# Optimization experiments

Hardware: AMD Instinct MI355X
Metric: run time of the kernel (lower is better)

The kernel has to match this reference:

```python
import jax, jax.numpy as jnp
import numpy as np

B, N, E, FIN, FOUT = 4, 50000, 800000, 128, 64
ALPHA = 0.2  # LeakyReLU negative slope
NEG_BIG = -9e15


def setup_inputs() -> dict:
    key = jax.random.key(0)
    kx, kw, ka, ksrc, kdst = jax.random.split(key, 5)
    X = jax.random.normal(kx, (B, N, FIN), dtype=jnp.float32)
    W = jax.random.normal(kw, (FIN, FOUT), dtype=jnp.float32) * 0.1
    a = jax.random.normal(ka, (1, 2 * FOUT), dtype=jnp.float32) * 0.1
    # edges [B,2,E]; guarantee every row (destination of aggregation) has >=1 edge
    # so e_rowsum > 0 (mirrors real adjacency which has self-loops / connectivity).
    src_rand = jax.random.randint(ksrc, (B, E - N), 0, N, dtype=jnp.int32)
    src = jnp.concatenate(
        [jnp.broadcast_to(jnp.arange(N, dtype=jnp.int32), (B, N)), src_rand], axis=1
    )
    dst = jax.random.randint(kdst, (B, E), 0, N, dtype=jnp.int32)
    edges = jnp.stack([src, dst], axis=1)  # [B,2,E]
    return {"X": X, "edges": edges, "W": W, "a": a}


def _per_graph(x, edge, W, a):
    # x: [N,FIN], edge: [2,E]
    h = x @ W                                   # [N,FOUT]
    a1, a2 = a[0, :FOUT], a[0, FOUT:]           # split a . concat(h_i,h_j)
    s = (h @ a1)[edge[0]] + (h @ a2)[edge[1]]   # [E] attention logits
    edge_e = jnp.exp(-jax.nn.leaky_relu(s, ALPHA))          # [E]
    rowsum = jax.ops.segment_sum(edge_e, edge[0], num_segments=N)  # [N]
    msg = edge_e[:, None] * h[edge[1]]          # [E,FOUT]
    h_prime = jax.ops.segment_sum(msg, edge[0], num_segments=N)    # [N,FOUT]
    h_prime = h_prime / rowsum[:, None]
    h_prime = jnp.where(jnp.isnan(h_prime), jnp.float32(NEG_BIG), h_prime)
    return h_prime


def reference(X, edges, W, a):
    out = jax.vmap(_per_graph, in_axes=(0, 0, None, None))(X, edges, W, a)  # [B,N,FOUT]
    return jax.nn.elu(out)  # concat=True path
```

## Files before the change

### kernel.cpp

```cpp
#include <hip/hip_runtime.h>

#define B_    4
#define N_    50000
#define E_    800000
#define FIN_  128
#define F_    64
#define BN_   (B_ * N_)
#define TOT_  (BN_ * F_)
#define BE_   (B_ * E_)
#define ALPHA_ 0.2f
#define NEG_BIG_ -9.0e15f

#define XS_STRIDE 132
#define GEMM_BLOCKS (BN_ / 64)
#define COUNT_BLOCKS (BE_ / 1024)

#define MAXDEG_ 28
#define OVFCAP_ 16384

__device__ __forceinline__ float bf2f(unsigned int u16) {
    union { unsigned int i; float f; } v;
    v.i = u16 << 16;
    return v.f;
}
__device__ __forceinline__ unsigned int f2bf(float f) {
    union { float f; unsigned int u; } v;
    v.f = f;
    unsigned int r = v.u + 0x7FFFu + ((v.u >> 16) & 1u);
    return r >> 16;
}

__global__ __launch_bounds__(256) void gemm_count_kernel(
    const float* __restrict__ X,
    const float* __restrict__ W,
    const float* __restrict__ a,
    const int* __restrict__ edges,
    unsigned short* __restrict__ hq,
    float* __restrict__ e1,
    float* __restrict__ e2,
    int* __restrict__ cnt,
    int* __restrict__ ell,
    int* __restrict__ ovfc,
    int2* __restrict__ ovf) {
    __shared__ float Wf[FIN_ * F_];
    __shared__ float Xs[64 * XS_STRIDE];

    const int tid = threadIdx.x;
    const int bid = blockIdx.x;

    if (bid & 1) {
        const int g  = (bid >> 1) * 256 + tid;
        const int ge = g * 4;
        const int b  = ge / E_;
        const int e  = ge - b * E_;
        const int4 s4 = *(const int4*)&edges[(size_t)b * 2 * E_ + e];
        const int4 d4 = *(const int4*)&edges[(size_t)b * 2 * E_ + E_ + e];
        const int ss[4] = { s4.x, s4.y, s4.z, s4.w };
        const int dd[4] = { d4.x, d4.y, d4.z, d4.w };
#pragma unroll
        for (int j = 0; j < 4; ++j) {
            const int gs = b * N_ + ss[j];
            const int r = atomicAdd(&cnt[gs], 1);
            if (r < MAXDEG_) {
                ell[gs * MAXDEG_ + r] = dd[j];
            } else {
                const int i = atomicAdd(ovfc, 1);
                if (i < OVFCAP_) ovf[i] = make_int2(gs, dd[j]);
            }
        }
        return;
    }

    const float4* Wg = (const float4*)W;
    for (int i = tid; i < 2048; i += 256)
        ((float4*)Wf)[i] = Wg[i];

    const int row0 = (bid >> 1) * 64;
    const float4* Xg = (const float4*)(X + (size_t)row0 * FIN_);
    for (int i = tid; i < 2048; i += 256) {
        const int r = i >> 5;
        const int c = i & 31;
        float4 v = Xg[i];
        *(float4*)&Xs[r * XS_STRIDE + c * 4] = v;
    }
    __syncthreads();

    const int cg = tid & 15;
    const int rg = tid >> 4;

    float acc[4][4] = {};
#pragma unroll 4
    for (int k = 0; k < FIN_; ++k) {
        const float4 wv = *(const float4*)&Wf[k * F_ + cg * 4];
        float xr[4];
#pragma unroll
        for (int j = 0; j < 4; ++j)
            xr[j] = Xs[(rg * 4 + j) * XS_STRIDE + k];
#pragma unroll
        for (int j = 0; j < 4; ++j) {
            acc[j][0] += xr[j] * wv.x;
            acc[j][1] += xr[j] * wv.y;
            acc[j][2] += xr[j] * wv.z;
            acc[j][3] += xr[j] * wv.w;
        }
    }

    float a1v[4], a2v[4];
#pragma unroll
    for (int i = 0; i < 4; ++i) {
        a1v[i] = a[cg * 4 + i];
        a2v[i] = a[F_ + cg * 4 + i];
    }

#pragma unroll
    for (int j = 0; j < 4; ++j) {
        const int row = row0 + rg * 4 + j;
        union { ushort4 v; unsigned short s[4]; } st;
#pragma unroll
        for (int i = 0; i < 4; ++i) st.s[i] = (unsigned short)f2bf(acc[j][i]);
        *(ushort4*)&hq[(size_t)row * F_ + cg * 4] = st.v;

        float p1 = acc[j][0] * a1v[0] + acc[j][1] * a1v[1] +
                   acc[j][2] * a1v[2] + acc[j][3] * a1v[3];
        float p2 = acc[j][0] * a2v[0] + acc[j][1] * a2v[1] +
                   acc[j][2] * a2v[2] + acc[j][3] * a2v[3];
#pragma unroll
        for (int m = 8; m >= 1; m >>= 1) {
            p1 += __shfl_xor(p1, m);
            p2 += __shfl_xor(p2, m);
        }
        if (cg == 0) { e1[row] = p1; e2[row] = p2; }
    }
}

__global__ __launch_bounds__(256) void gather_kernel(
    const int* __restrict__ cnt,
    const int* __restrict__ ell,
    const int* __restrict__ ovfc,
    const int2* __restrict__ ovf,
    const float* __restrict__ e1,
    const float* __restrict__ e2,
    const uint4* __restrict__ hq4,
    float* __restrict__ out) {
    const int tid = threadIdx.x;
    const int lane = tid & 63;
    const int grp = lane >> 3;
    const int sub = lane & 7;
    const int gs = (int)((blockIdx.x * 256 + tid) >> 6);
    const int b = gs / N_;
    const uint4* hb = hq4 + (size_t)b * N_ * 8;
    const float* e2b = e2 + b * N_;
    const int cv = cnt[gs];
    const float e1s = e1[gs];
    const int deg = cv < MAXDEG_ ? cv : MAXDEG_;
    const int base = gs * MAXDEG_;

    const bool v0 = grp < deg;
    const bool v1 = grp + 8 < deg;
    const bool v2 = grp + 16 < deg;
    const bool v3 = (grp < 4) && (grp + 24 < deg);
    const int d0 = ell[base + grp];
    const int d1 = ell[base + grp + 8];
    const int d2 = ell[base + grp + 16];
    const int d3 = (grp < 4) ? ell[base + grp + 24] : 0;

    float a0 = 0.f, a1 = 0.f, a2 = 0.f, a3 = 0.f;
    float a4 = 0.f, a5 = 0.f, a6 = 0.f, a7 = 0.f, rs = 0.f;

#define GAT_SLOT(vld, dv)                                              \
    if (vld) {                                                         \
        const float sv = e1s + e2b[dv];                                \
        const float lr = sv > 0.0f ? sv : ALPHA_ * sv;                 \
        const float wt = __expf(-lr);                                  \
        const uint4 p = hb[(size_t)(dv) * 8 + sub];                    \
        a0 += wt * bf2f(p.x & 0xFFFFu); a1 += wt * bf2f(p.x >> 16);    \
        a2 += wt * bf2f(p.y & 0xFFFFu); a3 += wt * bf2f(p.y >> 16);    \
        a4 += wt * bf2f(p.z & 0xFFFFu); a5 += wt * bf2f(p.z >> 16);    \
        a6 += wt * bf2f(p.w & 0xFFFFu); a7 += wt * bf2f(p.w >> 16);    \
        rs += wt;                                                      \
    }

    GAT_SLOT(v0, d0)
    GAT_SLOT(v1, d1)
    GAT_SLOT(v2, d2)
    GAT_SLOT(v3, d3)
#undef GAT_SLOT

    if (cv > MAXDEG_) {
        int no = *ovfc;
        if (no > OVFCAP_) no = OVFCAP_;
        for (int i = 0; i < no; ++i) {
            const int2 t = ovf[i];
            if (t.x == gs) {
                const float sv = e1s + e2b[t.y];
                const float lr = sv > 0.0f ? sv : ALPHA_ * sv;
                const float wt = __expf(-lr);
                if (grp == 0) {
                    const uint4 p = hb[(size_t)t.y * 8 + sub];
                    a0 += wt * bf2f(p.x & 0xFFFFu); a1 += wt * bf2f(p.x >> 16);
                    a2 += wt * bf2f(p.y & 0xFFFFu); a3 += wt * bf2f(p.y >> 16);
                    a4 += wt * bf2f(p.z & 0xFFFFu); a5 += wt * bf2f(p.z >> 16);
                    a6 += wt * bf2f(p.w & 0xFFFFu); a7 += wt * bf2f(p.w >> 16);
                    rs += wt;
                }
            }
        }
    }

#pragma unroll
    for (int m = 8; m <= 32; m <<= 1) {
        a0 += __shfl_xor(a0, m); a1 += __shfl_xor(a1, m);
        a2 += __shfl_xor(a2, m); a3 += __shfl_xor(a3, m);
        a4 += __shfl_xor(a4, m); a5 += __shfl_xor(a5, m);
        a6 += __shfl_xor(a6, m); a7 += __shfl_xor(a7, m);
        rs += __shfl_xor(rs, m);
    }

    if (grp == 0) {
        float v[8] = { a0 / rs, a1 / rs, a2 / rs, a3 / rs,
                       a4 / rs, a5 / rs, a6 / rs, a7 / rs };
        float o[8];
#pragma unroll
        for (int j = 0; j < 8; ++j) {
            float x = v[j];
            if (x != x) x = NEG_BIG_;
            o[j] = x > 0.0f ? x : (__expf(x) - 1.0f);
        }
        float* po = &out[(size_t)gs * F_ + sub * 8];
        *(float4*)&po[0] = make_float4(o[0], o[1], o[2], o[3]);
        *(float4*)&po[4] = make_float4(o[4], o[5], o[6], o[7]);
    }
}

extern "C" void kernel_launch(void* const* d_in, const int* in_sizes, int n_in,
                              void* d_out, int out_size, void* d_ws, size_t ws_size,
                              hipStream_t stream) {
    const float* X = (const float*)d_in[0];
    const int* edges = (const int*)d_in[1];
    const float* W = (const float*)d_in[2];
    const float* a = (const float*)d_in[3];
    float* out = (float*)d_out;

    float* e1 = (float*)d_ws;
    float* e2 = e1 + BN_;
    unsigned short* hq = (unsigned short*)(e2 + BN_);
    int* cnt = (int*)(hq + (size_t)BN_ * F_);
    int* ovfc = cnt + BN_;
    int2* ovf = (int2*)(ovfc + 4);
    int* ell = (int*)(ovf + OVFCAP_);

    (void)hipMemsetAsync(cnt, 0, (size_t)(BN_ + 4) * sizeof(int), stream);

    gemm_count_kernel<<<GEMM_BLOCKS + COUNT_BLOCKS, 256, 0, stream>>>(
        X, W, a, edges, hq, e1, e2, cnt, ell, ovfc, ovf);
    gather_kernel<<<BN_ / 4, 256, 0, stream>>>(
        cnt, ell, ovfc, ovf, e1, e2, (const uint4*)hq, out);
}
```

Before: 427.4 us.

## Store ELL adjacency as 16-bit indices and issue gather loads unconditionally

The ELL neighbor list is narrowed from int to unsigned short, since N fits in 16 bits, which halves its write and read traffic. The ELL buffer is now zero-filled by the memset so that unused slots point to node 0. The gather kernel then loads all four slots and their h rows without branching and masks the weights to zero. The count path issues its four atomics back to back. In exchange, the memset grows (about 11 MB) and the gather makes extra useless loads for empty slots.

```diff
diff --git a/kernel.cpp b/kernel.cpp
--- a/kernel.cpp
+++ b/kernel.cpp
@@ -39,7 +39,7 @@
     float* __restrict__ e1,
     float* __restrict__ e2,
     int* __restrict__ cnt,
-    int* __restrict__ ell,
+    unsigned short* __restrict__ ell,
     int* __restrict__ ovfc,
     int2* __restrict__ ovf) {
     __shared__ float Wf[FIN_ * F_];
@@ -55,17 +55,21 @@
         const int e  = ge - b * E_;
         const int4 s4 = *(const int4*)&edges[(size_t)b * 2 * E_ + e];
         const int4 d4 = *(const int4*)&edges[(size_t)b * 2 * E_ + E_ + e];
-        const int ss[4] = { s4.x, s4.y, s4.z, s4.w };
+        const int gsv[4] = { b * N_ + s4.x, b * N_ + s4.y,
+                             b * N_ + s4.z, b * N_ + s4.w };
         const int dd[4] = { d4.x, d4.y, d4.z, d4.w };
+        int r[4];
+        r[0] = atomicAdd(&cnt[gsv[0]], 1);
+        r[1] = atomicAdd(&cnt[gsv[1]], 1);
+        r[2] = atomicAdd(&cnt[gsv[2]], 1);
+        r[3] = atomicAdd(&cnt[gsv[3]], 1);
 #pragma unroll
         for (int j = 0; j < 4; ++j) {
-            const int gs = b * N_ + ss[j];
-            const int r = atomicAdd(&cnt[gs], 1);
-            if (r < MAXDEG_) {
-                ell[gs * MAXDEG_ + r] = dd[j];
+            if (r[j] < MAXDEG_) {
+                ell[(size_t)gsv[j] * MAXDEG_ + r[j]] = (unsigned short)dd[j];
             } else {
                 const int i = atomicAdd(ovfc, 1);
-                if (i < OVFCAP_) ovf[i] = make_int2(gs, dd[j]);
+                if (i < OVFCAP_) ovf[i] = make_int2(gsv[j], dd[j]);
             }
         }
         return;
@@ -133,9 +137,20 @@
     }
 }
 
+struct Acc9 {
+    float a0, a1, a2, a3, a4, a5, a6, a7, rs;
+    __device__ __forceinline__ void add(float wt, const uint4& p) {
+        a0 += wt * bf2f(p.x & 0xFFFFu); a1 += wt * bf2f(p.x >> 16);
+        a2 += wt * bf2f(p.y & 0xFFFFu); a3 += wt * bf2f(p.y >> 16);
+        a4 += wt * bf2f(p.z & 0xFFFFu); a5 += wt * bf2f(p.z >> 16);
+        a6 += wt * bf2f(p.w & 0xFFFFu); a7 += wt * bf2f(p.w >> 16);
+        rs += wt;
+    }
+};
+
 __global__ __launch_bounds__(256) void gather_kernel(
     const int* __restrict__ cnt,
-    const int* __restrict__ ell,
+    const unsigned short* __restrict__ ell,
     const int* __restrict__ ovfc,
     const int2* __restrict__ ovf,
     const float* __restrict__ e1,
@@ -152,39 +167,37 @@
     const float* e2b = e2 + b * N_;
     const int cv = cnt[gs];
     const float e1s = e1[gs];
-    const int deg = cv < MAXDEG_ ? cv : MAXDEG_;
-    const int base = gs * MAXDEG_;
-
-    const bool v0 = grp < deg;
-    const bool v1 = grp + 8 < deg;
-    const bool v2 = grp + 16 < deg;
-    const bool v3 = (grp < 4) && (grp + 24 < deg);
-    const int d0 = ell[base + grp];
-    const int d1 = ell[base + grp + 8];
-    const int d2 = ell[base + grp + 16];
-    const int d3 = (grp < 4) ? ell[base + grp + 24] : 0;
-
-    float a0 = 0.f, a1 = 0.f, a2 = 0.f, a3 = 0.f;
-    float a4 = 0.f, a5 = 0.f, a6 = 0.f, a7 = 0.f, rs = 0.f;
-
-#define GAT_SLOT(vld, dv)                                              \
-    if (vld) {                                                         \
-        const float sv = e1s + e2b[dv];                                \
-        const float lr = sv > 0.0f ? sv : ALPHA_ * sv;                 \
-        const float wt = __expf(-lr);                                  \
-        const uint4 p = hb[(size_t)(dv) * 8 + sub];                    \
-        a0 += wt * bf2f(p.x & 0xFFFFu); a1 += wt * bf2f(p.x >> 16);    \
-        a2 += wt * bf2f(p.y & 0xFFFFu); a3 += wt * bf2f(p.y >> 16);    \
-        a4 += wt * bf2f(p.z & 0xFFFFu); a5 += wt * bf2f(p.z >> 16);    \
-        a6 += wt * bf2f(p.w & 0xFFFFu); a7 += wt * bf2f(p.w >> 16);    \
-        rs += wt;                                                      \
-    }
-
-    GAT_SLOT(v0, d0)
-    GAT_SLOT(v1, d1)
-    GAT_SLOT(v2, d2)
-    GAT_SLOT(v3, d3)
-#undef GAT_SLOT
+    const unsigned short* eb = ell + (size_t)gs * MAXDEG_;
+
+    const int d0 = eb[grp];
+    const int d1 = eb[grp + 8];
+    const int d2 = eb[grp + 16];
+    const int d3 = (grp < 4) ? (int)eb[grp + 24] : 0;
+
+    const uint4 p0 = hb[(size_t)d0 * 8 + sub];
+    const uint4 p1 = hb[(size_t)d1 * 8 + sub];
+    const uint4 p2 = hb[(size_t)d2 * 8 + sub];
+    const uint4 p3 = hb[(size_t)d3 * 8 + sub];
+    const float s0 = e1s + e2b[d0];
+    const float s1 = e1s + e2b[d1];
+    const float s2 = e1s + e2b[d2];
+    const float s3 = e1s + e2b[d3];
+
+    const int dm = cv < MAXDEG_ ? cv : MAXDEG_;
+    float w0 = __expf(-(s0 > 0.0f ? s0 : ALPHA_ * s0));
+    float w1 = __expf(-(s1 > 0.0f ? s1 : ALPHA_ * s1));
+    float w2 = __expf(-(s2 > 0.0f ? s2 : ALPHA_ * s2));
+    float w3 = __expf(-(s3 > 0.0f ? s3 : ALPHA_ * s3));
+    w0 = (grp < dm) ? w0 : 0.0f;
+    w1 = (grp + 8 < dm) ? w1 : 0.0f;
+    w2 = (grp + 16 < dm) ? w2 : 0.0f;
+    w3 = (grp + 24 < dm) ? w3 : 0.0f;
+
+    Acc9 ac = {};
+    ac.add(w0, p0);
+    ac.add(w1, p1);
+    ac.add(w2, p2);
+    ac.add(w3, p3);
 
     if (cv > MAXDEG_) {
         int no = *ovfc;
@@ -197,11 +210,7 @@
                 const float wt = __expf(-lr);
                 if (grp == 0) {
                     const uint4 p = hb[(size_t)t.y * 8 + sub];
-                    a0 += wt * bf2f(p.x & 0xFFFFu); a1 += wt * bf2f(p.x >> 16);
-                    a2 += wt * bf2f(p.y & 0xFFFFu); a3 += wt * bf2f(p.y >> 16);
-                    a4 += wt * bf2f(p.z & 0xFFFFu); a5 += wt * bf2f(p.z >> 16);
-                    a6 += wt * bf2f(p.w & 0xFFFFu); a7 += wt * bf2f(p.w >> 16);
-                    rs += wt;
+                    ac.add(wt, p);
                 }
             }
         }
@@ -209,16 +218,17 @@
 
 #pragma unroll
     for (int m = 8; m <= 32; m <<= 1) {
-        a0 += __shfl_xor(a0, m); a1 += __shfl_xor(a1, m);
-        a2 += __shfl_xor(a2, m); a3 += __shfl_xor(a3, m);
-        a4 += __shfl_xor(a4, m); a5 += __shfl_xor(a5, m);
-        a6 += __shfl_xor(a6, m); a7 += __shfl_xor(a7, m);
-        rs += __shfl_xor(rs, m);
+        ac.a0 += __shfl_xor(ac.a0, m); ac.a1 += __shfl_xor(ac.a1, m);
+        ac.a2 += __shfl_xor(ac.a2, m); ac.a3 += __shfl_xor(ac.a3, m);
+        ac.a4 += __shfl_xor(ac.a4, m); ac.a5 += __shfl_xor(ac.a5, m);
+        ac.a6 += __shfl_xor(ac.a6, m); ac.a7 += __shfl_xor(ac.a7, m);
+        ac.rs += __shfl_xor(ac.rs, m);
     }
 
     if (grp == 0) {
-        float v[8] = { a0 / rs, a1 / rs, a2 / rs, a3 / rs,
-                       a4 / rs, a5 / rs, a6 / rs, a7 / rs };
+        const float rs = ac.rs;
+        float v[8] = { ac.a0 / rs, ac.a1 / rs, ac.a2 / rs, ac.a3 / rs,
+                       ac.a4 / rs, ac.a5 / rs, ac.a6 / rs, ac.a7 / rs };
         float o[8];
 #pragma unroll
         for (int j = 0; j < 8; ++j) {
@@ -246,10 +256,12 @@
     unsigned short* hq = (unsigned short*)(e2 + BN_);
     int* cnt = (int*)(hq + (size_t)BN_ * F_);
     int* ovfc = cnt + BN_;
-    int2* ovf = (int2*)(ovfc + 4);
-    int* ell = (int*)(ovf + OVFCAP_);
-
-    (void)hipMemsetAsync(cnt, 0, (size_t)(BN_ + 4) * sizeof(int), stream);
+    unsigned short* ell = (unsigned short*)(ovfc + 4);
+    int2* ovf = (int2*)(ell + (size_t)BN_ * MAXDEG_ + 8);
+
+    const size_t zbytes = (size_t)BN_ * sizeof(int) + 4 * sizeof(int) +
+                          ((size_t)BN_ * MAXDEG_ + 8) * sizeof(unsigned short);
+    (void)hipMemsetAsync(cnt, 0, zbytes, stream);
 
     gemm_count_kernel<<<GEMM_BLOCKS + COUNT_BLOCKS, 256, 0, stream>>>(
         X, W, a, edges, hq, e1, e2, cnt, ell, ovfc, ovf);
```

After: 435.0 us. No clear change (+1.8%).
